# Optimization experiments

Hardware: AMD Instinct MI355X
Metric: run time of the kernel (lower is better)

Reference implementation:

```python
import jax, jax.numpy as jnp
import numpy as np

B, T, P, C, H = 2, 2048, 2048, 1024, 16  # batch, new tokens, cached tokens, n_embd, n_head
HD = C // H  # head_dim = 64


def setup_inputs() -> dict:
    key = jax.random.key(0)
    ks = jax.random.split(key, 5)
    return {
        "x": jax.random.normal(ks[0], (B, T, C), dtype=jnp.float32),
        "k_cache": jax.random.normal(ks[1], (B, P, C), dtype=jnp.float32),
        "v_cache": jax.random.normal(ks[2], (B, P, C), dtype=jnp.float32),
        "W_attn": jax.random.normal(ks[3], (C, 3 * C), dtype=jnp.float32) * 0.02,
        "W_proj": jax.random.normal(ks[4], (C, C), dtype=jnp.float32) * 0.02,
    }


def reference(x, k_cache, v_cache, W_attn, W_proj):
    # c_attn (no bias): qkv projection, then split into q, k_rem, v_rem
    qkv = x @ W_attn                      # [B, T, 3C]
    q, k_rem, v_rem = jnp.split(qkv, 3, axis=2)
    # KV-cache concat along time
    k_full = jnp.concatenate([k_cache, k_rem], axis=1)  # [B, S, C], S = P + T
    v_full = jnp.concatenate([v_cache, v_rem], axis=1)
    S = P + T
    # reshape to heads
    qh = q.reshape(B, T, H, HD).transpose(0, 2, 1, 3)       # [B, H, T, HD]
    kh = k_full.reshape(B, S, H, HD).transpose(0, 2, 1, 3)  # [B, H, S, HD]
    vh = v_full.reshape(B, S, H, HD).transpose(0, 2, 1, 3)  # [B, H, S, HD]
    # full attention matrix (module explicitly disables flash)
    att = jnp.einsum("bhqd,bhkd->bhqk", qh, kh) * (1.0 / np.sqrt(HD))  # [B,H,T,S]
    # cache-offset causal mask: query global position = P + i attends to key j <= P + i
    mask = jnp.arange(S)[None, :] <= (P + jnp.arange(T))[:, None]  # [T, S]
    att = jnp.where(mask[None, None], att, -jnp.inf)
    att = jax.nn.softmax(att, axis=-1)
    # dropout p=0.0 (inference) -> no-op
    y = jnp.einsum("bhqk,bhkd->bhqd", att, vh)  # [B, H, T, HD]
    y = y.transpose(0, 2, 1, 3).reshape(B, T, C)
    y = y @ W_proj  # c_proj, no bias; resid dropout p=0 -> no-op
    return (y, k_full, v_full)
```

## Files before the change

kernel.cpp:

```cpp
#include <hip/hip_runtime.h>

#define BB 2
#define TT 2048
#define PP 2048
#define CC 1024
#define HH 16
#define SS 4096

typedef unsigned short u16;
typedef __attribute__((ext_vector_type(8))) short s16x8;
typedef __attribute__((ext_vector_type(4))) float f32x4;
typedef __attribute__((ext_vector_type(4))) unsigned short u16x4;

#define QSCALE 0.18033688011112042f

__device__ __forceinline__ u16 f2bf(float f) {
  unsigned u = __float_as_uint(f);
  u += 0x7fff + ((u >> 16) & 1);
  return (u16)(u >> 16);
}

__global__ __launch_bounds__(256) void cvt_f32_bf16(const float* __restrict__ src,
                                                    u16* __restrict__ dst) {
  size_t i = ((size_t)blockIdx.x * 256 + threadIdx.x) * 4;
  f32x4 v = *(const f32x4*)(src + i);
  u16x4 o = { f2bf(v[0]), f2bf(v[1]), f2bf(v[2]), f2bf(v[3]) };
  *(u16x4*)(dst + i) = o;
}

__global__ __launch_bounds__(256) void transpose_w_bf16(const float* __restrict__ src,
                                                        u16* __restrict__ dst,
                                                        int rows, int cols) {
  __shared__ float tile[64][65];
  int r0 = blockIdx.y * 64, c0 = blockIdx.x * 64;
  int tx = threadIdx.x & 63, ty = threadIdx.x >> 6;
#pragma unroll
  for (int i = 0; i < 16; i++) {
    int r = ty + i * 4;
    tile[r][tx] = src[(size_t)(r0 + r) * cols + c0 + tx];
  }
  __syncthreads();
#pragma unroll
  for (int i = 0; i < 16; i++) {
    int cc = ty + i * 4;
    dst[(size_t)(c0 + cc) * rows + r0 + tx] = f2bf(tile[tx][cc]);
  }
}

__global__ __launch_bounds__(256) void cache_copy(const float* __restrict__ kc,
                                                  const float* __restrict__ vc,
                                                  float* __restrict__ kf,
                                                  float* __restrict__ vf,
                                                  u16* __restrict__ kb) {
  size_t flat = ((size_t)blockIdx.x * 256 + threadIdx.x) * 4;
  int b = (int)(flat >> 21);
  size_t dsto = flat + (size_t)b * (TT * CC);
  f32x4 kv = *(const f32x4*)(kc + flat);
  f32x4 vv = *(const f32x4*)(vc + flat);
  *(f32x4*)(kf + dsto) = kv;
  *(f32x4*)(vf + dsto) = vv;
  u16x4 k4 = { f2bf(kv[0]), f2bf(kv[1]), f2bf(kv[2]), f2bf(kv[3]) };
  *(u16x4*)(kb + dsto) = k4;
}

__global__ __launch_bounds__(256) void vT_cache_kernel(const float* __restrict__ vc,
                                                       u16* __restrict__ vTb) {
  __shared__ float tile[64][65];
  int bh = blockIdx.y, b = bh >> 4, h = bh & 15;
  int p0 = blockIdx.x * 64;
  int tx = threadIdx.x & 63, ty = threadIdx.x >> 6;
#pragma unroll
  for (int i = 0; i < 16; i++) {
    int p = ty + i * 4;
    tile[p][tx] = vc[(size_t)(b * PP + p0 + p) * CC + h * 64 + tx];
  }
  __syncthreads();
#pragma unroll
  for (int i = 0; i < 16; i++) {
    int d = ty + i * 4;
    vTb[(size_t)((b * HH + h) * 64 + d) * SS + p0 + tx] = f2bf(tile[tx][d]);
  }
}

__global__ __launch_bounds__(256) void vT_rem_kernel(const float* __restrict__ vf,
                                                     u16* __restrict__ vTb) {
  __shared__ float tile[64][65];
  int bh = blockIdx.y, b = bh >> 4, h = bh & 15;
  int p0 = blockIdx.x * 64;
  int tx = threadIdx.x & 63, ty = threadIdx.x >> 6;
#pragma unroll
  for (int i = 0; i < 16; i++) {
    int p = ty + i * 4;
    tile[p][tx] = vf[(size_t)(b * SS + PP + p0 + p) * CC + h * 64 + tx];
  }
  __syncthreads();
#pragma unroll
  for (int i = 0; i < 16; i++) {
    int d = ty + i * 4;
    vTb[(size_t)((b * HH + h) * 64 + d) * SS + PP + p0 + tx] = f2bf(tile[tx][d]);
  }
}

__global__ __launch_bounds__(256) void gemm_bt(const u16* __restrict__ A,
                                               const u16* __restrict__ BT,
                                               int N, int mode,
                                               float* __restrict__ out0,
                                               u16* __restrict__ qb,
                                               float* __restrict__ kf,
                                               u16* __restrict__ kb,
                                               float* __restrict__ vf) {
  __shared__ u16 As[128 * 72];
  __shared__ u16 Bs[128 * 72];
  const int m0 = blockIdx.y * 128, n0 = blockIdx.x * 128;
  const int tid = threadIdx.x, lane = tid & 63, wave = tid >> 6;
  const int wm = wave & 1, wn = wave >> 1;
  const int c = lane & 15, quad = lane >> 4;
  const int chunk = tid & 7, rp = tid >> 3;

  f32x4 acc[4][4] = {};

  for (int k0 = 0; k0 < 1024; k0 += 64) {
#pragma unroll
    for (int it = 0; it < 4; it++) {
      int r = it * 32 + rp;
      *(s16x8*)&As[r * 72 + chunk * 8] =
          *(const s16x8*)(A + (size_t)(m0 + r) * 1024 + k0 + chunk * 8);
      *(s16x8*)&Bs[r * 72 + chunk * 8] =
          *(const s16x8*)(BT + (size_t)(n0 + r) * 1024 + k0 + chunk * 8);
    }
    __syncthreads();
#pragma unroll
    for (int kc = 0; kc < 64; kc += 32) {
      s16x8 af[4], bf[4];
#pragma unroll
      for (int i = 0; i < 4; i++) {
        af[i] = *(const s16x8*)&As[(wm * 64 + i * 16 + c) * 72 + kc + quad * 8];
        bf[i] = *(const s16x8*)&Bs[(wn * 64 + i * 16 + c) * 72 + kc + quad * 8];
      }
#pragma unroll
      for (int mi = 0; mi < 4; mi++)
#pragma unroll
        for (int ni = 0; ni < 4; ni++)
          acc[mi][ni] = __builtin_amdgcn_mfma_f32_16x16x32_bf16(af[mi], bf[ni], acc[mi][ni], 0, 0, 0);
    }
    __syncthreads();
  }

#pragma unroll
  for (int mi = 0; mi < 4; mi++) {
#pragma unroll
    for (int ni = 0; ni < 4; ni++) {
      f32x4 v = acc[mi][ni];
      int gmb = m0 + wm * 64 + mi * 16 + quad * 4;
      int gn = n0 + wn * 64 + ni * 16 + c;
      if (mode == 0) {
#pragma unroll
        for (int r = 0; r < 4; r++)
          out0[(size_t)(gmb + r) * N + gn] = v[r];
      } else {
        int region = n0 >> 10;
        if (region == 0) {
#pragma unroll
          for (int r = 0; r < 4; r++)
            qb[(size_t)(gmb + r) * 1024 + gn] = f2bf(v[r] * QSCALE);
        } else if (region == 1) {
          int ccol = gn - 1024;
#pragma unroll
          for (int r = 0; r < 4; r++) {
            int gm = gmb + r, b = gm >> 11, t = gm & 2047;
            size_t off = (size_t)b * (SS * CC) + (size_t)(PP + t) * CC + ccol;
            kf[off] = v[r];
            kb[off] = f2bf(v[r]);
          }
        } else {
          int ccol = gn - 2048;
#pragma unroll
          for (int r = 0; r < 4; r++) {
            int gm = gmb + r, b = gm >> 11, t = gm & 2047;
            vf[(size_t)b * (SS * CC) + (size_t)(PP + t) * CC + ccol] = v[r];
          }
        }
      }
    }
  }
}

__global__ __launch_bounds__(256) void attn_kernel(const u16* __restrict__ qb,
                                                   const u16* __restrict__ kb,
                                                   const u16* __restrict__ vT,
                                                   u16* __restrict__ yb) {
  __shared__ u16 Ks[64 * 72];
  __shared__ u16 Vs[80 * 72];
  __shared__ u16 Ps[4][32 * 72];
  const int bh = blockIdx.y, b = bh >> 4, h = bh & 15;
  const int qt = gridDim.x - 1 - blockIdx.x;
  const int q0 = qt * 128;
  const int tid = threadIdx.x, lane = tid & 63, wave = tid >> 6;
  const int c = lane & 15, quad = lane >> 4;

  for (int i = tid; i < 16 * 72; i += 256)
    Vs[64 * 72 + i] = (i < 72) ? (u16)0x3F80 : (u16)0;
  __syncthreads();
  const s16x8 ones0 = *(const s16x8*)&Vs[(64 + c) * 72 + quad * 8];
  const s16x8 ones1 = *(const s16x8*)&Vs[(64 + c) * 72 + 32 + quad * 8];

  s16x8 qf[2][2];
#pragma unroll
  for (int st = 0; st < 2; st++)
#pragma unroll
    for (int kc = 0; kc < 2; kc++) {
      int qr = q0 + wave * 32 + st * 16 + c;
      qf[st][kc] = *(const s16x8*)(qb + (size_t)(b * TT + qr) * 1024 + h * 64 + kc * 32 + quad * 8);
    }

  f32x4 o[2][5] = {};
  float m = -1e30f;

  const int s_end = PP + q0 + 128;
  const int chunk = tid & 7, rp = tid >> 3;

  for (int s0 = 0; s0 < s_end; s0 += 64) {
#pragma unroll
    for (int it = 0; it < 2; it++) {
      int r = it * 32 + rp;
      *(s16x8*)&Ks[r * 72 + chunk * 8] =
          *(const s16x8*)(kb + (size_t)(b * SS + s0 + r) * 1024 + h * 64 + chunk * 8);
      *(s16x8*)&Vs[r * 72 + chunk * 8] =
          *(const s16x8*)(vT + (size_t)((b * HH + h) * 64 + r) * SS + s0 + chunk * 8);
    }
    __syncthreads();

    f32x4 sc[2][4];
#pragma unroll
    for (int nt = 0; nt < 4; nt++) {
      s16x8 kf0 = *(const s16x8*)&Ks[(nt * 16 + c) * 72 + quad * 8];
      s16x8 kf1 = *(const s16x8*)&Ks[(nt * 16 + c) * 72 + 32 + quad * 8];
#pragma unroll
      for (int st = 0; st < 2; st++) {
        f32x4 z = { 0.f, 0.f, 0.f, 0.f };
        z = __builtin_amdgcn_mfma_f32_16x16x32_bf16(qf[st][0], kf0, z, 0, 0, 0);
        z = __builtin_amdgcn_mfma_f32_16x16x32_bf16(qf[st][1], kf1, z, 0, 0, 0);
        sc[st][nt] = z;
      }
    }
    const int diag = s0 - (PP + q0);
    if (diag >= 0) {
#pragma unroll
      for (int st = 0; st < 2; st++)
#pragma unroll
        for (int nt = 0; nt < 4; nt++) {
          int col = nt * 16 + c + diag;
#pragma unroll
          for (int r = 0; r < 4; r++) {
            int rq = wave * 32 + st * 16 + quad * 4 + r;
            if (col > rq) sc[st][nt][r] = -1e30f;
          }
        }
    }

    float lm = -1e30f;
#pragma unroll
    for (int st = 0; st < 2; st++)
#pragma unroll
      for (int nt = 0; nt < 4; nt++)
        lm = fmaxf(lm, fmaxf(fmaxf(sc[st][nt][0], sc[st][nt][1]),
                             fmaxf(sc[st][nt][2], sc[st][nt][3])));
#pragma unroll
    for (int off = 1; off < 64; off <<= 1)
      lm = fmaxf(lm, __shfl_xor(lm, off, 64));
    if (lm > m) {
      float alpha = __builtin_amdgcn_exp2f(m - lm);
      m = lm;
#pragma unroll
      for (int st = 0; st < 2; st++)
#pragma unroll
        for (int dt = 0; dt < 5; dt++)
#pragma unroll
          for (int r = 0; r < 4; r++) o[st][dt][r] *= alpha;
    }

    u16* Pw = Ps[wave];
#pragma unroll
    for (int st = 0; st < 2; st++)
#pragma unroll
      for (int nt = 0; nt < 4; nt++)
#pragma unroll
        for (int r = 0; r < 4; r++)
          Pw[(st * 16 + quad * 4 + r) * 72 + nt * 16 + c] =
              f2bf(__builtin_amdgcn_exp2f(sc[st][nt][r] - m));
    s16x8 pa[2][2];
#pragma unroll
    for (int st = 0; st < 2; st++) {
      pa[st][0] = *(const s16x8*)&Pw[(st * 16 + c) * 72 + quad * 8];
      pa[st][1] = *(const s16x8*)&Pw[(st * 16 + c) * 72 + 32 + quad * 8];
    }
#pragma unroll
    for (int dt = 0; dt < 4; dt++) {
      s16x8 vb0 = *(const s16x8*)&Vs[(dt * 16 + c) * 72 + quad * 8];
      s16x8 vb1 = *(const s16x8*)&Vs[(dt * 16 + c) * 72 + 32 + quad * 8];
#pragma unroll
      for (int st = 0; st < 2; st++) {
        o[st][dt] = __builtin_amdgcn_mfma_f32_16x16x32_bf16(pa[st][0], vb0, o[st][dt], 0, 0, 0);
        o[st][dt] = __builtin_amdgcn_mfma_f32_16x16x32_bf16(pa[st][1], vb1, o[st][dt], 0, 0, 0);
      }
    }
#pragma unroll
    for (int st = 0; st < 2; st++) {
      o[st][4] = __builtin_amdgcn_mfma_f32_16x16x32_bf16(pa[st][0], ones0, o[st][4], 0, 0, 0);
      o[st][4] = __builtin_amdgcn_mfma_f32_16x16x32_bf16(pa[st][1], ones1, o[st][4], 0, 0, 0);
    }
    __syncthreads();
  }

#pragma unroll
  for (int st = 0; st < 2; st++)
#pragma unroll
    for (int r = 0; r < 4; r++) {
      float l = __shfl(o[st][4][r], (lane & 48), 64);
      float inv = 1.0f / l;
      int qr = q0 + wave * 32 + st * 16 + quad * 4 + r;
#pragma unroll
      for (int dt = 0; dt < 4; dt++)
        yb[(size_t)(b * TT + qr) * 1024 + h * 64 + dt * 16 + c] = f2bf(o[st][dt][r] * inv);
    }
}

extern "C" void kernel_launch(void* const* d_in, const int* in_sizes, int n_in,
                              void* d_out, int out_size, void* d_ws, size_t ws_size,
                              hipStream_t stream) {
  const float* x       = (const float*)d_in[0];
  const float* k_cache = (const float*)d_in[1];
  const float* v_cache = (const float*)d_in[2];
  const float* W_attn  = (const float*)d_in[3];
  const float* W_proj  = (const float*)d_in[4];

  float* out_y = (float*)d_out;
  float* out_k = out_y + (size_t)BB * TT * CC;
  float* out_v = out_k + (size_t)BB * SS * CC;

  u16* xb  = (u16*)d_ws;
  u16* WaT = xb  + 4194304;
  u16* WpT = WaT + 3145728;
  u16* qb  = WpT + 1048576;
  u16* kb  = qb  + 4194304;
  u16* vT  = kb  + 8388608;
  u16* yb  = vT  + 8388608;

  cvt_f32_bf16<<<dim3(4096), dim3(256), 0, stream>>>(x, xb);
  transpose_w_bf16<<<dim3(48, 16), dim3(256), 0, stream>>>(W_attn, WaT, 1024, 3072);
  transpose_w_bf16<<<dim3(16, 16), dim3(256), 0, stream>>>(W_proj, WpT, 1024, 1024);
  cache_copy<<<dim3(4096), dim3(256), 0, stream>>>(k_cache, v_cache, out_k, out_v, kb);
  vT_cache_kernel<<<dim3(32, 32), dim3(256), 0, stream>>>(v_cache, vT);
  gemm_bt<<<dim3(24, 32), dim3(256), 0, stream>>>(xb, WaT, 3072, 1, nullptr, qb, out_k, kb, out_v);
  vT_rem_kernel<<<dim3(32, 32), dim3(256), 0, stream>>>(out_v, vT);
  attn_kernel<<<dim3(16, 32), dim3(256), 0, stream>>>(qb, kb, vT, yb);
  gemm_bt<<<dim3(8, 32), dim3(256), 0, stream>>>(yb, WpT, 1024, 0, out_y, nullptr, nullptr, nullptr, nullptr);
}
```

Baseline: 366.1 us.

## Use 8 waves per attention block with register-prefetched K/V tiles

The attention kernel now runs 512 threads per block, with each wave owning 16 query rows instead of 32. This halves per-wave register state and raises the number of waves available to hide latency. The next K/V tile is prefetched into registers while the current tile is being computed. The rescale is skipped unless the running max grows by more than 8, which cuts the exp2 and multiply work. MFMA sections are also wrapped in s_setprio. Risks are fewer MFMAs per LDS load of K/V and a lazy max that could overflow bf16/fp32 for large score growth.

```diff
diff --git a/kernel.cpp b/kernel.cpp
--- a/kernel.cpp
+++ b/kernel.cpp
@@ -185,144 +185,132 @@
   }
 }
 
-__global__ __launch_bounds__(256) void attn_kernel(const u16* __restrict__ qb,
-                                                   const u16* __restrict__ kb,
-                                                   const u16* __restrict__ vT,
-                                                   u16* __restrict__ yb) {
+__global__ __launch_bounds__(512, 4) void attn_kernel(const u16* __restrict__ qb,
+                                                      const u16* __restrict__ kb,
+                                                      const u16* __restrict__ vT,
+                                                      u16* __restrict__ yb) {
   __shared__ u16 Ks[64 * 72];
   __shared__ u16 Vs[80 * 72];
-  __shared__ u16 Ps[4][32 * 72];
+  __shared__ u16 Ps[8][16 * 72];
   const int bh = blockIdx.y, b = bh >> 4, h = bh & 15;
   const int qt = gridDim.x - 1 - blockIdx.x;
   const int q0 = qt * 128;
   const int tid = threadIdx.x, lane = tid & 63, wave = tid >> 6;
   const int c = lane & 15, quad = lane >> 4;
-
-  for (int i = tid; i < 16 * 72; i += 256)
+  const int chunk = tid & 7, rp = tid >> 3;
+
+  const int s_end = PP + q0 + 128;
+
+  const u16* kptr = kb + (size_t)(b * SS + rp) * 1024 + h * 64 + chunk * 8;
+  const u16* vptr = vT + (size_t)((b * HH + h) * 64 + rp) * SS + chunk * 8;
+
+  s16x8 kreg = *(const s16x8*)kptr;
+  s16x8 vreg = *(const s16x8*)vptr;
+
+  for (int i = tid; i < 16 * 72; i += 512)
     Vs[64 * 72 + i] = (i < 72) ? (u16)0x3F80 : (u16)0;
   __syncthreads();
   const s16x8 ones0 = *(const s16x8*)&Vs[(64 + c) * 72 + quad * 8];
   const s16x8 ones1 = *(const s16x8*)&Vs[(64 + c) * 72 + 32 + quad * 8];
 
-  s16x8 qf[2][2];
-#pragma unroll
-  for (int st = 0; st < 2; st++)
-#pragma unroll
-    for (int kc = 0; kc < 2; kc++) {
-      int qr = q0 + wave * 32 + st * 16 + c;
-      qf[st][kc] = *(const s16x8*)(qb + (size_t)(b * TT + qr) * 1024 + h * 64 + kc * 32 + quad * 8);
-    }
-
-  f32x4 o[2][5] = {};
+  s16x8 qf[2];
+  {
+    int qr = q0 + wave * 16 + c;
+    qf[0] = *(const s16x8*)(qb + (size_t)(b * TT + qr) * 1024 + h * 64 + quad * 8);
+    qf[1] = *(const s16x8*)(qb + (size_t)(b * TT + qr) * 1024 + h * 64 + 32 + quad * 8);
+  }
+
+  f32x4 o[5] = {};
   float m = -1e30f;
-
-  const int s_end = PP + q0 + 128;
-  const int chunk = tid & 7, rp = tid >> 3;
+  u16* Pw = Ps[wave];
 
   for (int s0 = 0; s0 < s_end; s0 += 64) {
-#pragma unroll
-    for (int it = 0; it < 2; it++) {
-      int r = it * 32 + rp;
-      *(s16x8*)&Ks[r * 72 + chunk * 8] =
-          *(const s16x8*)(kb + (size_t)(b * SS + s0 + r) * 1024 + h * 64 + chunk * 8);
-      *(s16x8*)&Vs[r * 72 + chunk * 8] =
-          *(const s16x8*)(vT + (size_t)((b * HH + h) * 64 + r) * SS + s0 + chunk * 8);
-    }
+    *(s16x8*)&Ks[rp * 72 + chunk * 8] = kreg;
+    *(s16x8*)&Vs[rp * 72 + chunk * 8] = vreg;
     __syncthreads();
 
-    f32x4 sc[2][4];
+    if (s0 + 64 < s_end) {
+      kptr += 64 * 1024;
+      vptr += 64;
+      kreg = *(const s16x8*)kptr;
+      vreg = *(const s16x8*)vptr;
+    }
+
+    f32x4 sc[4];
+    __builtin_amdgcn_s_setprio(1);
 #pragma unroll
     for (int nt = 0; nt < 4; nt++) {
       s16x8 kf0 = *(const s16x8*)&Ks[(nt * 16 + c) * 72 + quad * 8];
       s16x8 kf1 = *(const s16x8*)&Ks[(nt * 16 + c) * 72 + 32 + quad * 8];
-#pragma unroll
-      for (int st = 0; st < 2; st++) {
-        f32x4 z = { 0.f, 0.f, 0.f, 0.f };
-        z = __builtin_amdgcn_mfma_f32_16x16x32_bf16(qf[st][0], kf0, z, 0, 0, 0);
-        z = __builtin_amdgcn_mfma_f32_16x16x32_bf16(qf[st][1], kf1, z, 0, 0, 0);
-        sc[st][nt] = z;
-      }
-    }
+      f32x4 z = { 0.f, 0.f, 0.f, 0.f };
+      z = __builtin_amdgcn_mfma_f32_16x16x32_bf16(qf[0], kf0, z, 0, 0, 0);
+      z = __builtin_amdgcn_mfma_f32_16x16x32_bf16(qf[1], kf1, z, 0, 0, 0);
+      sc[nt] = z;
+    }
+    __builtin_amdgcn_s_setprio(0);
+
     const int diag = s0 - (PP + q0);
     if (diag >= 0) {
 #pragma unroll
-      for (int st = 0; st < 2; st++)
-#pragma unroll
-        for (int nt = 0; nt < 4; nt++) {
-          int col = nt * 16 + c + diag;
-#pragma unroll
-          for (int r = 0; r < 4; r++) {
-            int rq = wave * 32 + st * 16 + quad * 4 + r;
-            if (col > rq) sc[st][nt][r] = -1e30f;
-          }
+      for (int nt = 0; nt < 4; nt++) {
+        int col = nt * 16 + c + diag;
+#pragma unroll
+        for (int r = 0; r < 4; r++) {
+          int rq = wave * 16 + quad * 4 + r;
+          if (col > rq) sc[nt][r] = -1e30f;
         }
+      }
     }
 
     float lm = -1e30f;
 #pragma unroll
-    for (int st = 0; st < 2; st++)
-#pragma unroll
-      for (int nt = 0; nt < 4; nt++)
-        lm = fmaxf(lm, fmaxf(fmaxf(sc[st][nt][0], sc[st][nt][1]),
-                             fmaxf(sc[st][nt][2], sc[st][nt][3])));
+    for (int nt = 0; nt < 4; nt++)
+      lm = fmaxf(lm, fmaxf(fmaxf(sc[nt][0], sc[nt][1]),
+                           fmaxf(sc[nt][2], sc[nt][3])));
 #pragma unroll
     for (int off = 1; off < 64; off <<= 1)
       lm = fmaxf(lm, __shfl_xor(lm, off, 64));
-    if (lm > m) {
+    if (lm > m + 8.0f) {
       float alpha = __builtin_amdgcn_exp2f(m - lm);
       m = lm;
 #pragma unroll
-      for (int st = 0; st < 2; st++)
-#pragma unroll
-        for (int dt = 0; dt < 5; dt++)
-#pragma unroll
-          for (int r = 0; r < 4; r++) o[st][dt][r] *= alpha;
-    }
-
-    u16* Pw = Ps[wave];
-#pragma unroll
-    for (int st = 0; st < 2; st++)
-#pragma unroll
-      for (int nt = 0; nt < 4; nt++)
-#pragma unroll
-        for (int r = 0; r < 4; r++)
-          Pw[(st * 16 + quad * 4 + r) * 72 + nt * 16 + c] =
-              f2bf(__builtin_amdgcn_exp2f(sc[st][nt][r] - m));
-    s16x8 pa[2][2];
-#pragma unroll
-    for (int st = 0; st < 2; st++) {
-      pa[st][0] = *(const s16x8*)&Pw[(st * 16 + c) * 72 + quad * 8];
-      pa[st][1] = *(const s16x8*)&Pw[(st * 16 + c) * 72 + 32 + quad * 8];
-    }
+      for (int dt = 0; dt < 5; dt++)
+#pragma unroll
+        for (int r = 0; r < 4; r++) o[dt][r] *= alpha;
+    }
+
+#pragma unroll
+    for (int nt = 0; nt < 4; nt++)
+#pragma unroll
+      for (int r = 0; r < 4; r++)
+        Pw[(quad * 4 + r) * 72 + nt * 16 + c] =
+            f2bf(__builtin_amdgcn_exp2f(sc[nt][r] - m));
+    s16x8 pa0 = *(const s16x8*)&Pw[c * 72 + quad * 8];
+    s16x8 pa1 = *(const s16x8*)&Pw[c * 72 + 32 + quad * 8];
+
+    __builtin_amdgcn_s_setprio(1);
 #pragma unroll
     for (int dt = 0; dt < 4; dt++) {
       s16x8 vb0 = *(const s16x8*)&Vs[(dt * 16 + c) * 72 + quad * 8];
       s16x8 vb1 = *(const s16x8*)&Vs[(dt * 16 + c) * 72 + 32 + quad * 8];
-#pragma unroll
-      for (int st = 0; st < 2; st++) {
-        o[st][dt] = __builtin_amdgcn_mfma_f32_16x16x32_bf16(pa[st][0], vb0, o[st][dt], 0, 0, 0);
-        o[st][dt] = __builtin_amdgcn_mfma_f32_16x16x32_bf16(pa[st][1], vb1, o[st][dt], 0, 0, 0);
-      }
-    }
-#pragma unroll
-    for (int st = 0; st < 2; st++) {
-      o[st][4] = __builtin_amdgcn_mfma_f32_16x16x32_bf16(pa[st][0], ones0, o[st][4], 0, 0, 0);
-      o[st][4] = __builtin_amdgcn_mfma_f32_16x16x32_bf16(pa[st][1], ones1, o[st][4], 0, 0, 0);
-    }
+      o[dt] = __builtin_amdgcn_mfma_f32_16x16x32_bf16(pa0, vb0, o[dt], 0, 0, 0);
+      o[dt] = __builtin_amdgcn_mfma_f32_16x16x32_bf16(pa1, vb1, o[dt], 0, 0, 0);
+    }
+    o[4] = __builtin_amdgcn_mfma_f32_16x16x32_bf16(pa0, ones0, o[4], 0, 0, 0);
+    o[4] = __builtin_amdgcn_mfma_f32_16x16x32_bf16(pa1, ones1, o[4], 0, 0, 0);
+    __builtin_amdgcn_s_setprio(0);
     __syncthreads();
   }
 
 #pragma unroll
-  for (int st = 0; st < 2; st++)
-#pragma unroll
-    for (int r = 0; r < 4; r++) {
-      float l = __shfl(o[st][4][r], (lane & 48), 64);
-      float inv = 1.0f / l;
-      int qr = q0 + wave * 32 + st * 16 + quad * 4 + r;
-#pragma unroll
-      for (int dt = 0; dt < 4; dt++)
-        yb[(size_t)(b * TT + qr) * 1024 + h * 64 + dt * 16 + c] = f2bf(o[st][dt][r] * inv);
-    }
+  for (int r = 0; r < 4; r++) {
+    float l = __shfl(o[4][r], (lane & 48), 64);
+    float inv = 1.0f / l;
+    int qr = q0 + wave * 16 + quad * 4 + r;
+#pragma unroll
+    for (int dt = 0; dt < 4; dt++)
+      yb[(size_t)(b * TT + qr) * 1024 + h * 64 + dt * 16 + c] = f2bf(o[dt][r] * inv);
+  }
 }
 
 extern "C" void kernel_launch(void* const* d_in, const int* in_sizes, int n_in,
@@ -353,6 +341,6 @@
   vT_cache_kernel<<<dim3(32, 32), dim3(256), 0, stream>>>(v_cache, vT);
   gemm_bt<<<dim3(24, 32), dim3(256), 0, stream>>>(xb, WaT, 3072, 1, nullptr, qb, out_k, kb, out_v);
   vT_rem_kernel<<<dim3(32, 32), dim3(256), 0, stream>>>(out_v, vT);
-  attn_kernel<<<dim3(16, 32), dim3(256), 0, stream>>>(qb, kb, vT, yb);
+  attn_kernel<<<dim3(16, 32), dim3(512), 0, stream>>>(qb, kb, vT, yb);
   gemm_bt<<<dim3(8, 32), dim3(256), 0, stream>>>(yb, WpT, 1024, 0, out_y, nullptr, nullptr, nullptr, nullptr);
 }
```

Result: no change. 361.7 us (-1.2%).

## Load K/V fragments directly from global, drop LDS staging and block barriers

Applied to the files above, without the earlier changes.

The attention kernel no longer stages K and V tiles through shared memory. Each wave now reads its MFMA operands straight from global memory, which removes both __syncthreads per tile. Alongside that, it remaps blocks so heads are grouped per XCD for L2 reuse, builds the ones-vector for the row-sum in registers, XOR-swizzles the P buffer to avoid bank conflicts, adds s_setprio around MFMA phases, and rescales only when the max grows by more than 8 (lazy rescale). The trade-off is redundant global/L2 traffic, since all four waves read the same K/V, in exchange for fewer barriers and more occupancy.

```diff
diff --git a/kernel.cpp b/kernel.cpp
--- a/kernel.cpp
+++ b/kernel.cpp
@@ -185,24 +185,25 @@
   }
 }
 
-__global__ __launch_bounds__(256) void attn_kernel(const u16* __restrict__ qb,
-                                                   const u16* __restrict__ kb,
-                                                   const u16* __restrict__ vT,
-                                                   u16* __restrict__ yb) {
-  __shared__ u16 Ks[64 * 72];
-  __shared__ u16 Vs[80 * 72];
+__global__ __launch_bounds__(256, 2) void attn_kernel(const u16* __restrict__ qb,
+                                                      const u16* __restrict__ kb,
+                                                      const u16* __restrict__ vT,
+                                                      u16* __restrict__ yb) {
   __shared__ u16 Ps[4][32 * 72];
-  const int bh = blockIdx.y, b = bh >> 4, h = bh & 15;
-  const int qt = gridDim.x - 1 - blockIdx.x;
+  const int L = blockIdx.x;
+  const int xcd = L & 7, rest = L >> 3;
+  const int qt = 15 - (rest >> 2);
+  const int bh = (xcd << 2) | (rest & 3);
+  const int b = bh >> 4, h = bh & 15;
   const int q0 = qt * 128;
   const int tid = threadIdx.x, lane = tid & 63, wave = tid >> 6;
   const int c = lane & 15, quad = lane >> 4;
 
-  for (int i = tid; i < 16 * 72; i += 256)
-    Vs[64 * 72 + i] = (i < 72) ? (u16)0x3F80 : (u16)0;
-  __syncthreads();
-  const s16x8 ones0 = *(const s16x8*)&Vs[(64 + c) * 72 + quad * 8];
-  const s16x8 ones1 = *(const s16x8*)&Vs[(64 + c) * 72 + 32 + quad * 8];
+  const u16* kbase = kb + (size_t)b * (SS * CC) + h * 64;
+  const u16* vbase = vT + (size_t)bh * 64 * SS;
+
+  const short ov = (c == 0) ? (short)0x3F80 : (short)0;
+  const s16x8 ones = { ov, ov, ov, ov, ov, ov, ov, ov };
 
   s16x8 qf[2][2];
 #pragma unroll
@@ -215,26 +216,18 @@
 
   f32x4 o[2][5] = {};
   float m = -1e30f;
+  u16* Pw = Ps[wave];
 
   const int s_end = PP + q0 + 128;
-  const int chunk = tid & 7, rp = tid >> 3;
 
   for (int s0 = 0; s0 < s_end; s0 += 64) {
-#pragma unroll
-    for (int it = 0; it < 2; it++) {
-      int r = it * 32 + rp;
-      *(s16x8*)&Ks[r * 72 + chunk * 8] =
-          *(const s16x8*)(kb + (size_t)(b * SS + s0 + r) * 1024 + h * 64 + chunk * 8);
-      *(s16x8*)&Vs[r * 72 + chunk * 8] =
-          *(const s16x8*)(vT + (size_t)((b * HH + h) * 64 + r) * SS + s0 + chunk * 8);
-    }
-    __syncthreads();
-
     f32x4 sc[2][4];
+    __builtin_amdgcn_s_setprio(1);
 #pragma unroll
     for (int nt = 0; nt < 4; nt++) {
-      s16x8 kf0 = *(const s16x8*)&Ks[(nt * 16 + c) * 72 + quad * 8];
-      s16x8 kf1 = *(const s16x8*)&Ks[(nt * 16 + c) * 72 + 32 + quad * 8];
+      const u16* kr = kbase + (size_t)(s0 + nt * 16 + c) * CC + quad * 8;
+      s16x8 kf0 = *(const s16x8*)kr;
+      s16x8 kf1 = *(const s16x8*)(kr + 32);
 #pragma unroll
       for (int st = 0; st < 2; st++) {
         f32x4 z = { 0.f, 0.f, 0.f, 0.f };
@@ -243,6 +236,16 @@
         sc[st][nt] = z;
       }
     }
+    __builtin_amdgcn_s_setprio(0);
+
+    s16x8 va[4], vb[4];
+#pragma unroll
+    for (int dt = 0; dt < 4; dt++) {
+      const u16* vr = vbase + (size_t)(dt * 16 + c) * SS + s0 + quad * 8;
+      va[dt] = *(const s16x8*)vr;
+      vb[dt] = *(const s16x8*)(vr + 32);
+    }
+
     const int diag = s0 - (PP + q0);
     if (diag >= 0) {
 #pragma unroll
@@ -268,7 +271,7 @@
 #pragma unroll
     for (int off = 1; off < 64; off <<= 1)
       lm = fmaxf(lm, __shfl_xor(lm, off, 64));
-    if (lm > m) {
+    if (lm > m + 8.0f) {
       float alpha = __builtin_amdgcn_exp2f(m - lm);
       m = lm;
 #pragma unroll
@@ -279,37 +282,40 @@
           for (int r = 0; r < 4; r++) o[st][dt][r] *= alpha;
     }
 
-    u16* Pw = Ps[wave];
 #pragma unroll
     for (int st = 0; st < 2; st++)
 #pragma unroll
       for (int nt = 0; nt < 4; nt++)
 #pragma unroll
-        for (int r = 0; r < 4; r++)
-          Pw[(st * 16 + quad * 4 + r) * 72 + nt * 16 + c] =
+        for (int r = 0; r < 4; r++) {
+          int R = st * 16 + quad * 4 + r;
+          Pw[(R * 72 + nt * 16 + c) ^ (quad << 3)] =
               f2bf(__builtin_amdgcn_exp2f(sc[st][nt][r] - m));
+        }
     s16x8 pa[2][2];
 #pragma unroll
     for (int st = 0; st < 2; st++) {
-      pa[st][0] = *(const s16x8*)&Pw[(st * 16 + c) * 72 + quad * 8];
-      pa[st][1] = *(const s16x8*)&Pw[(st * 16 + c) * 72 + 32 + quad * 8];
-    }
+      int rbase = (st * 16 + c) * 72;
+      int key = (c >> 2) << 3;
+      pa[st][0] = *(const s16x8*)&Pw[(rbase + quad * 8) ^ key];
+      pa[st][1] = *(const s16x8*)&Pw[(rbase + 32 + quad * 8) ^ key];
+    }
+
+    __builtin_amdgcn_s_setprio(1);
 #pragma unroll
     for (int dt = 0; dt < 4; dt++) {
-      s16x8 vb0 = *(const s16x8*)&Vs[(dt * 16 + c) * 72 + quad * 8];
-      s16x8 vb1 = *(const s16x8*)&Vs[(dt * 16 + c) * 72 + 32 + quad * 8];
 #pragma unroll
       for (int st = 0; st < 2; st++) {
-        o[st][dt] = __builtin_amdgcn_mfma_f32_16x16x32_bf16(pa[st][0], vb0, o[st][dt], 0, 0, 0);
-        o[st][dt] = __builtin_amdgcn_mfma_f32_16x16x32_bf16(pa[st][1], vb1, o[st][dt], 0, 0, 0);
+        o[st][dt] = __builtin_amdgcn_mfma_f32_16x16x32_bf16(pa[st][0], va[dt], o[st][dt], 0, 0, 0);
+        o[st][dt] = __builtin_amdgcn_mfma_f32_16x16x32_bf16(pa[st][1], vb[dt], o[st][dt], 0, 0, 0);
       }
     }
 #pragma unroll
     for (int st = 0; st < 2; st++) {
-      o[st][4] = __builtin_amdgcn_mfma_f32_16x16x32_bf16(pa[st][0], ones0, o[st][4], 0, 0, 0);
-      o[st][4] = __builtin_amdgcn_mfma_f32_16x16x32_bf16(pa[st][1], ones1, o[st][4], 0, 0, 0);
-    }
-    __syncthreads();
+      o[st][4] = __builtin_amdgcn_mfma_f32_16x16x32_bf16(pa[st][0], ones, o[st][4], 0, 0, 0);
+      o[st][4] = __builtin_amdgcn_mfma_f32_16x16x32_bf16(pa[st][1], ones, o[st][4], 0, 0, 0);
+    }
+    __builtin_amdgcn_s_setprio(0);
   }
 
 #pragma unroll
@@ -353,6 +359,6 @@
   vT_cache_kernel<<<dim3(32, 32), dim3(256), 0, stream>>>(v_cache, vT);
   gemm_bt<<<dim3(24, 32), dim3(256), 0, stream>>>(xb, WaT, 3072, 1, nullptr, qb, out_k, kb, out_v);
   vT_rem_kernel<<<dim3(32, 32), dim3(256), 0, stream>>>(out_v, vT);
-  attn_kernel<<<dim3(16, 32), dim3(256), 0, stream>>>(qb, kb, vT, yb);
+  attn_kernel<<<dim3(512), dim3(256), 0, stream>>>(qb, kb, vT, yb);
   gemm_bt<<<dim3(8, 32), dim3(256), 0, stream>>>(yb, WpT, 1024, 0, out_y, nullptr, nullptr, nullptr, nullptr);
 }
```

Result: slower. 423.3 us (+15.6%).
